# Optimization experiments

Measured on AMD Instinct MI355X. Metric: run time of the kernel, lower is better.

Reference implementation:

```python
import jax, jax.numpy as jnp
import numpy as np

N, E, HID, H, L, R = 20000, 160000, 512, 8, 4, 128
DK = HID // H
SCALE = 1.0 / np.sqrt(DK)
EPS = 1e-5


def setup_inputs() -> dict:
    key = jax.random.key(0)
    ks = jax.random.split(key, 24)
    p = lambda i, shape: jax.random.normal(ks[i], shape, jnp.float32) * 0.02
    return {
        'x': jax.random.normal(ks[0], (N, HID), jnp.float32),
        'relations': jax.random.randint(ks[1], (E,), 0, R),
        'src': jax.random.randint(ks[2], (E,), 0, N),
        'dst': jax.random.randint(ks[3], (E,), 0, N),
        'rel_embed': p(4, (R, HID)),
        'Wq': p(5, (L, HID, HID)), 'bq': jnp.zeros((L, HID), jnp.float32),
        'Wk': p(6, (L, HID, HID)), 'bk': jnp.zeros((L, HID), jnp.float32),
        'Wv': p(7, (L, HID, HID)), 'bv': jnp.zeros((L, HID), jnp.float32),
        'Wo': p(8, (L, HID, HID)), 'bo': jnp.zeros((L, HID), jnp.float32),
        'W1': p(9, (L, HID, 4 * HID)), 'b1': jnp.zeros((L, 4 * HID), jnp.float32),
        'W2': p(10, (L, 4 * HID, HID)), 'b2': jnp.zeros((L, HID), jnp.float32),
        'ln1_g': jnp.ones((L, HID), jnp.float32), 'ln1_b': jnp.zeros((L, HID), jnp.float32),
        'ln2_g': jnp.ones((L, HID), jnp.float32), 'ln2_b': jnp.zeros((L, HID), jnp.float32),
    }


def _ln(x, g, b):
    m = x.mean(-1, keepdims=True)
    v = jnp.square(x - m).mean(-1, keepdims=True)
    return (x - m) * jax.lax.rsqrt(v + EPS) * g + b


def _layer(x, rh, src, dst, Wq, bq, Wk, bk, Wv, bv, Wo, bo, W1, b1, W2, b2, g1, bb1, g2, bb2):
    # rh: (E, H, DK) per-edge relation features
    q = (x @ Wq + bq).reshape(N, H, DK)
    k = (x @ Wk + bk).reshape(N, H, DK)
    v = (x @ Wv + bv).reshape(N, H, DK)
    # edge score: ((k_src + r) . q_dst) / sqrt(d_k)   -> (E, H)
    score = jnp.einsum('ehd,ehd->eh', k[src] + rh, q[dst]) * SCALE
    # segment softmax over incoming edges of each dst node
    smax = jax.ops.segment_max(score, dst, num_segments=N)
    smax = jnp.where(jnp.isfinite(smax), smax, 0.0)  # nodes with no in-edges
    ex = jnp.exp(score - smax[dst])                   # (E, H)
    z = jax.ops.segment_sum(ex, dst, num_segments=N)  # (N, H)
    wv = jax.ops.segment_sum(ex[:, :, None] * (v[src] + rh), dst, num_segments=N)  # (N, H, DK)
    o = wv / (z[:, :, None] + 1e-9)
    o = o.reshape(N, HID) @ Wo + bo
    h = _ln(x + o, g1, bb1)
    ff = jax.nn.relu(h @ W1 + b1) @ W2 + b2
    return _ln(h + ff, g2, bb2)


def reference(x, relations, src, dst, rel_embed, Wq, bq, Wk, bk, Wv, bv, Wo, bo, W1, b1, W2, b2, ln1_g, ln1_b, ln2_g, ln2_b):
    lg_x = rel_embed[relations]            # (E, HID), shared across layers
    rh = lg_x.reshape(E, H, DK)
    for i in range(L):
        x = _layer(x, rh, src, dst, Wq[i], bq[i], Wk[i], bk[i], Wv[i], bv[i],
                   Wo[i], bo[i], W1[i], b1[i], W2[i], b2[i],
                   ln1_g[i], ln1_b[i], ln2_g[i], ln2_b[i])
    return x
```

## Files before the change

kernel.cpp:

```cpp
#include <hip/hip_runtime.h>
#include <cstdint>
#include <cstddef>

#define N_NODES 20000
#define N_EDGES 160000
#define HIDDEN  512
#define NHEAD   8
#define HDK     64
#define NLAYER  4
#define FFDIM   2048
#define ATT_SCALE 0.125f
#define S1C 262144
#define S2C 1048576
#define WLYR (4 * S1C + 2 * S2C)

typedef float  f4  __attribute__((ext_vector_type(4)));
typedef short  s8v __attribute__((ext_vector_type(8)));
typedef __bf16 b8v __attribute__((ext_vector_type(8)));

template <typename V>
__device__ inline auto mfma_try(V a, V b, f4 c, int)
    -> decltype(__builtin_amdgcn_mfma_f32_16x16x32_bf16(a, b, c, 0, 0, 0)) {
  return __builtin_amdgcn_mfma_f32_16x16x32_bf16(a, b, c, 0, 0, 0);
}
template <typename V>
__device__ inline f4 mfma_try(V a, V b, f4 c, long) {
  return __builtin_amdgcn_mfma_f32_16x16x32_bf16(
      __builtin_bit_cast(b8v, a), __builtin_bit_cast(b8v, b), c, 0, 0, 0);
}
__device__ inline f4 mfma_bf16(s8v a, s8v b, f4 c) { return mfma_try(a, b, c, 0); }

__device__ __forceinline__ unsigned short f2bf(float f) {
  unsigned u = __builtin_bit_cast(unsigned, f);
  u += 0x7FFFu + ((u >> 16) & 1u);
  return (unsigned short)(u >> 16);
}
__device__ __forceinline__ float bf2f(unsigned short u) {
  return __builtin_bit_cast(float, (unsigned)u << 16);
}

#define GLOAD_LDS16(gp, lp)                                                   \
  __builtin_amdgcn_global_load_lds(                                           \
      (const __attribute__((address_space(1))) void*)(gp),                    \
      (__attribute__((address_space(3))) void*)(lp), 16, 0, 0)

__global__ void cast8_kernel(const float* __restrict__ in, unsigned short* __restrict__ out, int n8) {
  int i = blockIdx.x * blockDim.x + threadIdx.x;
  if (i < n8) {
    f4 a = ((const f4*)in)[i * 2];
    f4 b = ((const f4*)in)[i * 2 + 1];
    s8v o;
#pragma unroll
    for (int j = 0; j < 4; ++j) {
      o[j]     = (short)f2bf(a[j]);
      o[j + 4] = (short)f2bf(b[j]);
    }
    ((s8v*)out)[i] = o;
  }
}

__global__ void weight_prep_kernel(const float* __restrict__ Wq, const float* __restrict__ Wk,
                                   const float* __restrict__ Wv, const float* __restrict__ Wo_,
                                   const float* __restrict__ W1, const float* __restrict__ W2,
                                   const float* __restrict__ bq, const float* __restrict__ bk,
                                   const float* __restrict__ bv,
                                   unsigned short* __restrict__ wAll, float* __restrict__ bqkvAll) {
  int l = blockIdx.x / 3078;
  int id = blockIdx.x % 3078;
  unsigned short* wqkv = wAll + (size_t)l * WLYR;
  unsigned short* wo = wqkv + 3 * S1C;
  unsigned short* w1 = wo + S1C;
  unsigned short* w2 = w1 + S2C;
  if (id >= 3072) {
    int i = (id - 3072) * 256 + threadIdx.y * 32 + threadIdx.x;
    float* bqkv = bqkvAll + l * 1536;
    if (i < 512) bqkv[i] = bq[l * 512 + i];
    else if (i < 1024) bqkv[i] = bk[l * 512 + i - 512];
    else if (i < 1536) bqkv[i] = bv[l * 512 + i - 1024];
    return;
  }
  const float* in; unsigned short* out; int K, N, bx, by;
  if (id < 1024) {
    int m = id >> 8, t = id & 255;
    in = ((m == 0) ? Wq : (m == 1) ? Wk : (m == 2) ? Wv : Wo_) + (size_t)l * S1C;
    out = (m == 3) ? wo : wqkv + m * S1C;
    K = 512; N = 512; bx = t & 15; by = t >> 4;
  } else if (id < 2048) {
    int t = id - 1024;
    in = W1 + (size_t)l * S2C; out = w1; K = 512; N = 2048; bx = t & 63; by = t >> 6;
  } else {
    int t = id - 2048;
    in = W2 + (size_t)l * S2C; out = w2; K = 2048; N = 512; bx = t & 15; by = t >> 4;
  }
  __shared__ float t32[32][33];
  int tx = threadIdx.x, ty = threadIdx.y;
  int n0 = bx * 32, k0 = by * 32;
  int Kc = K >> 3;
#pragma unroll
  for (int i = 0; i < 32; i += 8)
    t32[ty + i][tx] = in[(size_t)(k0 + ty + i) * N + n0 + tx];
  __syncthreads();
#pragma unroll
  for (int i = 0; i < 32; i += 8) {
    int n = n0 + ty + i, k = k0 + tx;
    size_t idx = ((size_t)(n >> 4) * Kc + (k >> 3)) * 128 + (n & 15) * 8 + (k & 7);
    out[idx] = f2bf(t32[tx][ty + i]);
  }
}

#define BM 128
#define BN 128
#define BK 64

template <bool OBF16, bool SPLITB>
__global__ __launch_bounds__(256, SPLITB ? 4 : 3) void gemm_bf16(
    const unsigned short* __restrict__ A, const unsigned short* __restrict__ Bt,
    const float* __restrict__ bias, void* __restrict__ Cp,
    int M, int K, int N, int relu) {
  __shared__ __align__(16) unsigned short As[8192];
  int tid = threadIdx.x;
  int wave = tid >> 6, lane = tid & 63;
  int quad = lane >> 4, l16 = lane & 15;
  int wm = (wave >> 1) * 64, wn = (wave & 1) * 64;

  int T = gridDim.x * gridDim.y;
  int i = blockIdx.y * gridDim.x + blockIdx.x;
  int C = T >> 3;
  int w = (i < (C << 3)) ? ((i & 7) * C + (i >> 3)) : i;
  int bx = w % gridDim.x, by = w / gridDim.x;
  int m0 = by * BM, n0 = bx * BN;

  f4 acc[4][4];
#pragma unroll
  for (int i2 = 0; i2 < 4; ++i2)
#pragma unroll
    for (int j = 0; j < 4; ++j) acc[i2][j] = (f4){0.f, 0.f, 0.f, 0.f};

  int rbase = wave * 8 + (lane >> 3);
  int q8 = (lane & 7) ^ ((lane >> 3) & 7);
  const unsigned short* aptr[4];
#pragma unroll
  for (int j = 0; j < 4; ++j) {
    int r = j * 32 + rbase;
    int gm = m0 + r; if (gm >= M) gm = M - 1;
    aptr[j] = A + (size_t)gm * K + q8 * 8;
  }

  int Kc = K >> 3;
  const unsigned short* bbase = Bt + quad * 128 + l16 * 8;
  size_t nioff[4];
#pragma unroll
  for (int i2 = 0; i2 < 4; ++i2)
    nioff[i2] = ((size_t)((n0 >> 4) + (wn >> 4) + i2) * Kc) * 128;

  int nk = K >> 6;
  for (int ks = 0; ks < nk; ++ks) {
#pragma unroll
    for (int j = 0; j < 4; ++j)
      GLOAD_LDS16(aptr[j], &As[j * 2048 + wave * 512]);

    if constexpr (SPLITB) {
      s8v bfr[4];
#pragma unroll
      for (int i2 = 0; i2 < 4; ++i2)
        bfr[i2] = *(const s8v*)(bbase + nioff[i2] + (size_t)ks * 1024);
#pragma unroll
      for (int j = 0; j < 4; ++j) aptr[j] += BK;
      __syncthreads();
      {
        s8v af[4];
#pragma unroll
        for (int i2 = 0; i2 < 4; ++i2) {
          int ra = wm + i2 * 16 + l16;
          af[i2] = *(const s8v*)(&As[ra * 64 + (((quad) ^ (ra & 7)) * 8)]);
        }
#pragma unroll
        for (int mi = 0; mi < 4; ++mi)
#pragma unroll
          for (int ni = 0; ni < 4; ++ni)
            acc[mi][ni] = mfma_bf16(af[mi], bfr[ni], acc[mi][ni]);
      }
#pragma unroll
      for (int i2 = 0; i2 < 4; ++i2)
        bfr[i2] = *(const s8v*)(bbase + nioff[i2] + (size_t)ks * 1024 + 512);
      {
        s8v af[4];
#pragma unroll
        for (int i2 = 0; i2 < 4; ++i2) {
          int ra = wm + i2 * 16 + l16;
          af[i2] = *(const s8v*)(&As[ra * 64 + (((4 | quad) ^ (ra & 7)) * 8)]);
        }
#pragma unroll
        for (int mi = 0; mi < 4; ++mi)
#pragma unroll
          for (int ni = 0; ni < 4; ++ni)
            acc[mi][ni] = mfma_bf16(af[mi], bfr[ni], acc[mi][ni]);
      }
      __syncthreads();
    } else {
      s8v bfr[2][4];
#pragma unroll
      for (int s = 0; s < 2; ++s)
#pragma unroll
        for (int i2 = 0; i2 < 4; ++i2)
          bfr[s][i2] = *(const s8v*)(bbase + nioff[i2] + (size_t)ks * 1024 + s * 512);
#pragma unroll
      for (int j = 0; j < 4; ++j) aptr[j] += BK;
      __syncthreads();
#pragma unroll
      for (int s = 0; s < 2; ++s) {
        s8v af[4];
#pragma unroll
        for (int i2 = 0; i2 < 4; ++i2) {
          int ra = wm + i2 * 16 + l16;
          af[i2] = *(const s8v*)(&As[ra * 64 + ((((s << 2) | quad) ^ (ra & 7)) * 8)]);
        }
#pragma unroll
        for (int mi = 0; mi < 4; ++mi)
#pragma unroll
          for (int ni = 0; ni < 4; ++ni)
            acc[mi][ni] = mfma_bf16(af[mi], bfr[s][ni], acc[mi][ni]);
      }
      __syncthreads();
    }
  }

  if constexpr (OBF16) {
    unsigned short* Cs = As + wave * 1088;
    float bvv[4];
#pragma unroll
    for (int ni = 0; ni < 4; ++ni) bvv[ni] = bias[n0 + wn + ni * 16 + l16];
    int row_l = lane >> 2, cg = lane & 3;
#pragma unroll
    for (int mi = 0; mi < 4; ++mi) {
#pragma unroll
      for (int ni = 0; ni < 4; ++ni) {
#pragma unroll
        for (int r = 0; r < 4; ++r) {
          float val = acc[mi][ni][r] + bvv[ni];
          if (relu) val = fmaxf(val, 0.f);
          Cs[(quad * 4 + r) * 68 + ni * 16 + l16] = f2bf(val);
        }
      }
      s8v v0 = *(const s8v*)(&Cs[row_l * 68 + cg * 16]);
      s8v v1 = *(const s8v*)(&Cs[row_l * 68 + cg * 16 + 8]);
      int grow = m0 + wm + mi * 16 + row_l;
      if (grow < M) {
        unsigned short* cp = (unsigned short*)Cp + (size_t)grow * N + n0 + wn + cg * 16;
        *(s8v*)cp = v0;
        *(s8v*)(cp + 8) = v1;
      }
    }
  } else {
#pragma unroll
    for (int ni = 0; ni < 4; ++ni) {
      int col = n0 + wn + ni * 16 + l16;
      float bv = bias[col];
#pragma unroll
      for (int mi = 0; mi < 4; ++mi) {
#pragma unroll
        for (int r = 0; r < 4; ++r) {
          int row = m0 + wm + mi * 16 + quad * 4 + r;
          if (row < M) {
            float val = acc[mi][ni][r] + bv;
            if (relu) val = fmaxf(val, 0.f);
            ((float*)Cp)[(size_t)row * N + col] = val;
          }
        }
      }
    }
  }
}

__global__ __launch_bounds__(256, 4) void gemm_sm(
    const unsigned short* __restrict__ A, const unsigned short* __restrict__ Bt,
    const float* __restrict__ bias, unsigned short* __restrict__ Cp,
    int M, int K, int N, int relu) {
  __shared__ __align__(16) unsigned short As[4096];
  int tid = threadIdx.x;
  int wave = tid >> 6, lane = tid & 63;
  int quad = lane >> 4, l16 = lane & 15;
  int wn = wave * 32;

  int T = gridDim.x * gridDim.y;
  int i = blockIdx.y * gridDim.x + blockIdx.x;
  int C = T >> 3;
  int w = (i < (C << 3)) ? ((i & 7) * C + (i >> 3)) : i;
  int bx = w % gridDim.x, by = w / gridDim.x;
  int m0 = by * 64, n0 = bx * BN;

  f4 acc[4][2];
#pragma unroll
  for (int i2 = 0; i2 < 4; ++i2)
#pragma unroll
    for (int j = 0; j < 2; ++j) acc[i2][j] = (f4){0.f, 0.f, 0.f, 0.f};

  int rbase = wave * 8 + (lane >> 3);
  int q8 = (lane & 7) ^ ((lane >> 3) & 7);
  const unsigned short* aptr[2];
#pragma unroll
  for (int j = 0; j < 2; ++j) {
    int r = j * 32 + rbase;
    int gm = m0 + r; if (gm >= M) gm = M - 1;
    aptr[j] = A + (size_t)gm * K + q8 * 8;
  }

  int Kc = K >> 3;
  const unsigned short* bbase = Bt + quad * 128 + l16 * 8;
  size_t nioff[2];
#pragma unroll
  for (int i2 = 0; i2 < 2; ++i2)
    nioff[i2] = ((size_t)((n0 >> 4) + (wn >> 4) + i2) * Kc) * 128;

  int nk = K >> 6;
  for (int ks = 0; ks < nk; ++ks) {
#pragma unroll
    for (int j = 0; j < 2; ++j)
      GLOAD_LDS16(aptr[j], &As[j * 2048 + wave * 512]);
    s8v bfr[2][2];
#pragma unroll
    for (int s = 0; s < 2; ++s)
#pragma unroll
      for (int i2 = 0; i2 < 2; ++i2)
        bfr[s][i2] = *(const s8v*)(bbase + nioff[i2] + (size_t)ks * 1024 + s * 512);
#pragma unroll
    for (int j = 0; j < 2; ++j) aptr[j] += BK;
    __syncthreads();
#pragma unroll
    for (int s = 0; s < 2; ++s) {
      s8v af[4];
#pragma unroll
      for (int i2 = 0; i2 < 4; ++i2) {
        int ra = i2 * 16 + l16;
        af[i2] = *(const s8v*)(&As[ra * 64 + ((((s << 2) | quad) ^ (ra & 7)) * 8)]);
      }
#pragma unroll
      for (int mi = 0; mi < 4; ++mi)
#pragma unroll
        for (int ni = 0; ni < 2; ++ni)
          acc[mi][ni] = mfma_bf16(af[mi], bfr[s][ni], acc[mi][ni]);
    }
    __syncthreads();
  }

  unsigned short* Cs = As + wave * 576;
  float bvv[2];
#pragma unroll
  for (int ni = 0; ni < 2; ++ni) bvv[ni] = bias[n0 + wn + ni * 16 + l16];
  int row_l = lane >> 2, cg = lane & 3;
#pragma unroll
  for (int mi = 0; mi < 4; ++mi) {
#pragma unroll
    for (int ni = 0; ni < 2; ++ni)
#pragma unroll
      for (int r = 0; r < 4; ++r) {
        float val = acc[mi][ni][r] + bvv[ni];
        if (relu) val = fmaxf(val, 0.f);
        Cs[(quad * 4 + r) * 36 + ni * 16 + l16] = f2bf(val);
      }
    s8v v0 = *(const s8v*)(&Cs[row_l * 36 + cg * 8]);
    int grow = m0 + mi * 16 + row_l;
    if (grow < M) {
      unsigned short* cp = Cp + (size_t)grow * N + n0 + wn + cg * 8;
      *(s8v*)cp = v0;
    }
  }
}

__global__ void hist_kernel(const int* __restrict__ dst, int* __restrict__ cnt, int E) {
  int e = blockIdx.x * blockDim.x + threadIdx.x;
  if (e < E) atomicAdd(&cnt[dst[e]], 1);
}

__global__ void scan_blk_kernel(const int* __restrict__ cnt, int* __restrict__ incl,
                                int* __restrict__ bsum, int n) {
  __shared__ int sh[1024];
  int tid = threadIdx.x;
  int gi = blockIdx.x * 1024 + tid;
  int v = (gi < n) ? cnt[gi] : 0;
  sh[tid] = v;
  __syncthreads();
  for (int s = 1; s < 1024; s <<= 1) {
    int t = (tid >= s) ? sh[tid - s] : 0;
    __syncthreads();
    sh[tid] += t;
    __syncthreads();
  }
  if (gi < n) incl[gi] = sh[tid];
  if (tid == 1023) bsum[blockIdx.x] = sh[1023];
}

__global__ void scan_mid_kernel(const int* __restrict__ bsum, int* __restrict__ boff, int nb) {
  if (threadIdx.x == 0 && blockIdx.x == 0) {
    int run = 0;
    for (int i = 0; i < nb; ++i) { boff[i] = run; run += bsum[i]; }
    boff[nb] = run;
  }
}

__global__ void scan_fix_kernel(const int* __restrict__ incl, const int* __restrict__ boff,
                                int* __restrict__ offs, int n) {
  int gi = blockIdx.x * 1024 + threadIdx.x;
  if (gi < n) offs[gi + 1] = boff[blockIdx.x] + incl[gi];
  if (gi == 0) offs[0] = 0;
}

__global__ void scatter_kernel(const int* __restrict__ dst, const int* __restrict__ src,
                               const int* __restrict__ relations, const int* __restrict__ offs,
                               int* __restrict__ cursor, int* __restrict__ esrc,
                               int* __restrict__ erel, int E) {
  int e = blockIdx.x * blockDim.x + threadIdx.x;
  if (e < E) {
    int d = dst[e];
    int pos = offs[d] + atomicAdd(&cursor[d], 1);
    esrc[pos] = src[e];
    erel[pos] = relations[e];
  }
}

#define ATT_LOAD(j, kx, vx, rx) do {                                          \
    int sj = __shfl(si_l, (j), 64);                                           \
    int rj = __shfl(ri_l, (j), 64);                                           \
    kx = *(const s8v*)(k + (size_t)sj * STR + base);                          \
    vx = *(const s8v*)(v + (size_t)sj * STR + base);                          \
    rx = *(const s8v*)(relb + (size_t)rj * HIDDEN + base);                    \
  } while (0)

#define ATT_STEP(kc, vc, rc) do {                                             \
    float rf[8], p = 0.f;                                                     \
    _Pragma("unroll") for (int jj = 0; jj < 8; ++jj) {                        \
      rf[jj] = bf2f((unsigned short)kc[jj]);                                  \
      float rr = bf2f((unsigned short)rc[jj]);                                \
      p += (rf[jj] + rr) * qf[jj];                                            \
      rf[jj] = rr;                                                            \
    }                                                                         \
    p += __shfl_xor(p, 1, 64);                                                \
    p += __shfl_xor(p, 2, 64);                                                \
    p += __shfl_xor(p, 4, 64);                                                \
    p *= ATT_SCALE;                                                           \
    float mn = fmaxf(m, p);                                                   \
    float a = __expf(m - mn);                                                 \
    float wgt = __expf(p - mn);                                               \
    z = z * a + wgt;                                                          \
    _Pragma("unroll") for (int jj = 0; jj < 8; ++jj)                          \
      acc[jj] = acc[jj] * a + wgt * (bf2f((unsigned short)vc[jj]) + rf[jj]);  \
    m = mn;                                                                   \
  } while (0)

__global__ void edge_attn_kernel(const unsigned short* __restrict__ q,
                                 const unsigned short* __restrict__ k,
                                 const unsigned short* __restrict__ v,
                                 const unsigned short* __restrict__ relb,
                                 const int* __restrict__ offs,
                                 const int* __restrict__ esrc,
                                 const int* __restrict__ erel,
                                 unsigned short* __restrict__ o, int Nn, int STR) {
  int wid = (blockIdx.x * blockDim.x + threadIdx.x) >> 6;
  int lane = threadIdx.x & 63;
  if (wid >= Nn) return;
  int base = (lane >> 3) * HDK + (lane & 7) * 8;

  s8v qv = *(const s8v*)(q + (size_t)wid * STR + base);
  float qf[8];
#pragma unroll
  for (int j = 0; j < 8; ++j) qf[j] = bf2f((unsigned short)qv[j]);

  int beg = offs[wid], end = offs[wid + 1];
  float m = -1e30f, z = 0.f;
  float acc[8];
#pragma unroll
  for (int j = 0; j < 8; ++j) acc[j] = 0.f;

  for (int cbeg = beg; cbeg < end; cbeg += 64) {
    int cn = end - cbeg; if (cn > 64) cn = 64;
    int e = cbeg + lane;
    int si_l = 0, ri_l = 0;
    if (e < end) { si_l = esrc[e]; ri_l = erel[e]; }
    s8v kA = {}, vA = {}, rA = {};
    s8v kB = {}, vB = {}, rB = {};
    s8v kC = {}, vC = {}, rC = {};
    if (cn > 0) ATT_LOAD(0, kA, vA, rA);
    if (cn > 1) ATT_LOAD(1, kB, vB, rB);
    if (cn > 2) ATT_LOAD(2, kC, vC, rC);
    int j = 0;
    for (; j + 5 < cn; j += 3) {
      ATT_STEP(kA, vA, rA); ATT_LOAD(j + 3, kA, vA, rA);
      ATT_STEP(kB, vB, rB); ATT_LOAD(j + 4, kB, vB, rB);
      ATT_STEP(kC, vC, rC); ATT_LOAD(j + 5, kC, vC, rC);
    }
    int r = cn - j;
    if (r >= 1) ATT_STEP(kA, vA, rA);
    if (r >= 4) ATT_LOAD(j + 3, kA, vA, rA);
    if (r >= 2) ATT_STEP(kB, vB, rB);
    if (r >= 5) ATT_LOAD(j + 4, kB, vB, rB);
    if (r >= 3) ATT_STEP(kC, vC, rC);
    if (r >= 4) ATT_STEP(kA, vA, rA);
    if (r >= 5) ATT_STEP(kB, vB, rB);
  }

  float rz = 1.f / (z + 1e-9f);
  s8v ov;
#pragma unroll
  for (int j = 0; j < 8; ++j) ov[j] = (short)f2bf(acc[j] * rz);
  *(s8v*)(o + (size_t)wid * HIDDEN + base) = ov;
}

template <bool WF32>
__global__ void ln_kernel(const unsigned short* __restrict__ xp, const unsigned short* __restrict__ y,
                          const float* __restrict__ g, const float* __restrict__ b,
                          float* __restrict__ outf, unsigned short* __restrict__ outb, int Nn) {
  int wid = (blockIdx.x * blockDim.x + threadIdx.x) >> 6;
  int lane = threadIdx.x & 63;
  if (wid >= Nn) return;
  int base = lane * 8;
  s8v xv = *(const s8v*)(xp + (size_t)wid * HIDDEN + base);
  s8v yv = *(const s8v*)(y + (size_t)wid * HIDDEN + base);
  float vals[8];
  float sum = 0.f;
#pragma unroll
  for (int j = 0; j < 8; ++j) {
    vals[j] = bf2f((unsigned short)xv[j]) + bf2f((unsigned short)yv[j]);
    sum += vals[j];
  }
#pragma unroll
  for (int off = 32; off; off >>= 1) sum += __shfl_xor(sum, off, 64);
  float mean = sum * (1.f / 512.f);
  float sq = 0.f;
#pragma unroll
  for (int j = 0; j < 8; ++j) { float d = vals[j] - mean; sq += d * d; }
#pragma unroll
  for (int off = 32; off; off >>= 1) sq += __shfl_xor(sq, off, 64);
  float rstd = rsqrtf(sq * (1.f / 512.f) + 1e-5f);
  f4 gv0 = *(const f4*)(g + base);
  f4 gv1 = *(const f4*)(g + base + 4);
  f4 bv0 = *(const f4*)(b + base);
  f4 bv1 = *(const f4*)(b + base + 4);
  float ov_f[8];
#pragma unroll
  for (int j = 0; j < 4; ++j) {
    ov_f[j]     = (vals[j]     - mean) * rstd * gv0[j] + bv0[j];
    ov_f[j + 4] = (vals[j + 4] - mean) * rstd * gv1[j] + bv1[j];
  }
  s8v ov;
#pragma unroll
  for (int j = 0; j < 8; ++j) ov[j] = (short)f2bf(ov_f[j]);
  *(s8v*)(outb + (size_t)wid * HIDDEN + base) = ov;
  if constexpr (WF32) {
    f4 o0, o1;
#pragma unroll
    for (int j = 0; j < 4; ++j) { o0[j] = ov_f[j]; o1[j] = ov_f[j + 4]; }
    *(f4*)(outf + (size_t)wid * HIDDEN + base) = o0;
    *(f4*)(outf + (size_t)wid * HIDDEN + base + 4) = o1;
  }
}

extern "C" void kernel_launch(void* const* d_in, const int* in_sizes, int n_in,
                              void* d_out, int out_size, void* d_ws, size_t ws_size,
                              hipStream_t stream) {
  const float* x0        = (const float*)d_in[0];
  const int*   relations = (const int*)d_in[1];
  const int*   src       = (const int*)d_in[2];
  const int*   dst       = (const int*)d_in[3];
  const float* rel_embed = (const float*)d_in[4];
  const float* Wq = (const float*)d_in[5];  const float* bq = (const float*)d_in[6];
  const float* Wk = (const float*)d_in[7];  const float* bk = (const float*)d_in[8];
  const float* Wv = (const float*)d_in[9];  const float* bv = (const float*)d_in[10];
  const float* Wo = (const float*)d_in[11]; const float* bo = (const float*)d_in[12];
  const float* W1 = (const float*)d_in[13]; const float* b1 = (const float*)d_in[14];
  const float* W2 = (const float*)d_in[15]; const float* b2 = (const float*)d_in[16];
  const float* g1  = (const float*)d_in[17]; const float* bb1 = (const float*)d_in[18];
  const float* g2  = (const float*)d_in[19]; const float* bb2 = (const float*)d_in[20];
  float* xout = (float*)d_out;

  const size_t S1 = S1C;
  const size_t S2 = S2C;
  const size_t NH = (size_t)N_NODES * HIDDEN;

  unsigned short* wAll = (unsigned short*)d_ws;
  float* bqkvAll = (float*)(wAll + (size_t)NLAYER * WLYR);
  unsigned short* arena = (unsigned short*)(bqkvAll + NLAYER * 1536);
  unsigned short* qkvb = arena;
  unsigned short* ob   = arena + 3 * NH;
  unsigned short* ff1  = arena;
  unsigned short* proj = arena;
  unsigned short* hbb = arena + 4 * NH;
  unsigned short* xb  = hbb + NH;
  unsigned short* projb = xb + NH;
  unsigned short* relb  = projb + NH;
  int* cnt    = (int*)(relb + 65536);
  int* offs   = cnt + N_NODES;
  int* cursor = offs + N_NODES + 1;
  int* esrc   = cursor + N_NODES;
  int* erel   = esrc + N_EDGES;
  int* sincl  = erel + N_EDGES;
  int* sbsum  = sincl + 20480;
  int* sboff  = sbsum + 32;

  hipMemsetAsync(cnt, 0, N_NODES * sizeof(int), stream);
  hipMemsetAsync(cursor, 0, N_NODES * sizeof(int), stream);
  hist_kernel<<<(N_EDGES + 255) / 256, 256, 0, stream>>>(dst, cnt, N_EDGES);
  const int NB = (N_NODES + 1023) / 1024;
  scan_blk_kernel<<<NB, 1024, 0, stream>>>(cnt, sincl, sbsum, N_NODES);
  scan_mid_kernel<<<1, 64, 0, stream>>>(sbsum, sboff, NB);
  scan_fix_kernel<<<NB, 1024, 0, stream>>>(sincl, sboff, offs, N_NODES);
  scatter_kernel<<<(N_EDGES + 255) / 256, 256, 0, stream>>>(dst, src, relations, offs, cursor, esrc, erel, N_EDGES);
  cast8_kernel<<<(int)((NH / 8 + 255) / 256), 256, 0, stream>>>(x0, xb, (int)(NH / 8));
  cast8_kernel<<<32, 256, 0, stream>>>(rel_embed, relb, 8192);
  dim3 tb(32, 8);
  weight_prep_kernel<<<NLAYER * 3078, tb, 0, stream>>>(Wq, Wk, Wv, Wo, W1, W2, bq, bk, bv,
                                                       wAll, bqkvAll);

  const int MBc = (N_NODES + BM - 1) / BM;
  const int MBs = (N_NODES + 63) / 64;

  for (int l = 0; l < NLAYER; ++l) {
    unsigned short* wqkv = wAll + (size_t)l * WLYR;
    unsigned short* wo = wqkv + 3 * S1;
    unsigned short* w1 = wo + S1;
    unsigned short* w2 = w1 + S2;
    float* bqkv = bqkvAll + l * 1536;
    gemm_bf16<true, true><<<dim3(12, MBc), 256, 0, stream>>>(xb, wqkv, bqkv, qkvb, N_NODES, 512, 1536, 0);
    edge_attn_kernel<<<(N_NODES + 3) / 4, 256, 0, stream>>>(qkvb, qkvb + 512, qkvb + 1024,
                                                            relb, offs, esrc, erel, ob, N_NODES, 1536);
    gemm_sm<<<dim3(4, MBs), 256, 0, stream>>>(ob, wo, bo + l * 512, proj, N_NODES, 512, 512, 0);
    ln_kernel<false><<<N_NODES / 4, 256, 0, stream>>>(xb, proj, g1 + l * 512, bb1 + l * 512, nullptr, hbb, N_NODES);
    gemm_bf16<true, true><<<dim3(16, MBc), 256, 0, stream>>>(hbb, w1, b1 + l * 2048, ff1, N_NODES, 512, 2048, 1);
    gemm_sm<<<dim3(4, MBs), 256, 0, stream>>>(ff1, w2, b2 + l * 512, projb, N_NODES, 2048, 512, 0);
    if (l == NLAYER - 1)
      ln_kernel<true><<<N_NODES / 4, 256, 0, stream>>>(hbb, projb, g2 + l * 512, bb2 + l * 512, xout, xb, N_NODES);
    else
      ln_kernel<false><<<N_NODES / 4, 256, 0, stream>>>(hbb, projb, g2 + l * 512, bb2 + l * 512, nullptr, xb, N_NODES);
  }
}
```

Baseline: 1.162 ms.

## Write FF1 output in MFMA fragment layout and add LDS-free FF2 GEMM

The FF1 GEMM epilogue now writes its bf16 output directly in the 16x8 fragment-tiled layout that the MFMA operands expect. A new gemm_ff2 kernel reads A and B fragments straight from global memory with no LDS staging or barriers in the K loop, then uses LDS only for the output epilogue. This removes the shared-memory staging and synchronisation from the K=2048 down-projection. The trade-off is reliance on cache hits for global loads, with no double buffering. The output ragged edge depends on M being a multiple of 16.

```diff
diff --git a/kernel.cpp b/kernel.cpp
--- a/kernel.cpp
+++ b/kernel.cpp
@@ -112,7 +112,7 @@
 #define BN 128
 #define BK 64
 
-template <bool OBF16, bool SPLITB>
+template <bool OBF16, bool SPLITB, bool OUTFRAG>
 __global__ __launch_bounds__(256, SPLITB ? 4 : 3) void gemm_bf16(
     const unsigned short* __restrict__ A, const unsigned short* __restrict__ Bt,
     const float* __restrict__ bias, void* __restrict__ Cp,
@@ -225,7 +225,34 @@
     }
   }
 
-  if constexpr (OBF16) {
+  if constexpr (OUTFRAG) {
+    unsigned short* Cs = As + wave * 1024;
+    float bvv[4];
+#pragma unroll
+    for (int ni = 0; ni < 4; ++ni) bvv[ni] = bias[n0 + wn + ni * 16 + l16];
+    int Kc2 = N >> 3;
+    int c0 = (n0 + wn) >> 3;
+#pragma unroll
+    for (int mi = 0; mi < 4; ++mi) {
+#pragma unroll
+      for (int ni = 0; ni < 4; ++ni)
+#pragma unroll
+        for (int r = 0; r < 4; ++r) {
+          float val = acc[mi][ni][r] + bvv[ni];
+          if (relu) val = fmaxf(val, 0.f);
+          Cs[(ni * 2 + (l16 >> 3)) * 128 + (quad * 4 + r) * 8 + (l16 & 7)] = f2bf(val);
+        }
+      s8v v0 = *(const s8v*)(&Cs[lane * 16]);
+      s8v v1 = *(const s8v*)(&Cs[lane * 16 + 8]);
+      int gb = m0 + wm + mi * 16;
+      if (gb < M) {
+        unsigned short* cp = (unsigned short*)Cp +
+            ((size_t)(gb >> 4) * Kc2 + c0) * 128 + lane * 16;
+        *(s8v*)cp = v0;
+        *(s8v*)(cp + 8) = v1;
+      }
+    }
+  } else if constexpr (OBF16) {
     unsigned short* Cs = As + wave * 1088;
     float bvv[4];
 #pragma unroll
@@ -356,6 +383,79 @@
       for (int r = 0; r < 4; ++r) {
         float val = acc[mi][ni][r] + bvv[ni];
         if (relu) val = fmaxf(val, 0.f);
+        Cs[(quad * 4 + r) * 36 + ni * 16 + l16] = f2bf(val);
+      }
+    s8v v0 = *(const s8v*)(&Cs[row_l * 36 + cg * 8]);
+    int grow = m0 + mi * 16 + row_l;
+    if (grow < M) {
+      unsigned short* cp = Cp + (size_t)grow * N + n0 + wn + cg * 8;
+      *(s8v*)cp = v0;
+    }
+  }
+}
+
+__global__ __launch_bounds__(256, 4) void gemm_ff2(
+    const unsigned short* __restrict__ Af, const unsigned short* __restrict__ Bt,
+    const float* __restrict__ bias, unsigned short* __restrict__ Cp,
+    int M, int K, int N) {
+  __shared__ __align__(16) unsigned short Cs_s[2304];
+  int tid = threadIdx.x;
+  int wave = tid >> 6, lane = tid & 63;
+  int quad = lane >> 4, l16 = lane & 15;
+  int wn = wave * 32;
+
+  int T = gridDim.x * gridDim.y;
+  int i = blockIdx.y * gridDim.x + blockIdx.x;
+  int C = T >> 3;
+  int w = (i < (C << 3)) ? ((i & 7) * C + (i >> 3)) : i;
+  int bx = w % gridDim.x, by = w / gridDim.x;
+  int m0 = by * 64, n0 = bx * 128;
+
+  f4 acc[4][2];
+#pragma unroll
+  for (int i2 = 0; i2 < 4; ++i2)
+#pragma unroll
+    for (int j = 0; j < 2; ++j) acc[i2][j] = (f4){0.f, 0.f, 0.f, 0.f};
+
+  int Kc = K >> 3;
+  const unsigned short* ab = Af + ((size_t)(m0 >> 4) * Kc) * 128 + quad * 128 + l16 * 8;
+  const unsigned short* bbase = Bt + quad * 128 + l16 * 8;
+  size_t nioff[2];
+#pragma unroll
+  for (int i2 = 0; i2 < 2; ++i2)
+    nioff[i2] = ((size_t)((n0 >> 4) + (wn >> 4) + i2) * Kc) * 128;
+
+  int nk = K >> 6;
+  for (int ks = 0; ks < nk; ++ks) {
+#pragma unroll
+    for (int s = 0; s < 2; ++s) {
+      s8v af[4], bf[2];
+#pragma unroll
+      for (int i2 = 0; i2 < 4; ++i2)
+        af[i2] = *(const s8v*)(ab + ((size_t)i2 * Kc) * 128 + (size_t)ks * 1024 + s * 512);
+#pragma unroll
+      for (int i2 = 0; i2 < 2; ++i2)
+        bf[i2] = *(const s8v*)(bbase + nioff[i2] + (size_t)ks * 1024 + s * 512);
+#pragma unroll
+      for (int mi = 0; mi < 4; ++mi)
+#pragma unroll
+        for (int ni = 0; ni < 2; ++ni)
+          acc[mi][ni] = mfma_bf16(af[mi], bf[ni], acc[mi][ni]);
+    }
+  }
+
+  unsigned short* Cs = Cs_s + wave * 576;
+  float bvv[2];
+#pragma unroll
+  for (int ni = 0; ni < 2; ++ni) bvv[ni] = bias[n0 + wn + ni * 16 + l16];
+  int row_l = lane >> 2, cg = lane & 3;
+#pragma unroll
+  for (int mi = 0; mi < 4; ++mi) {
+#pragma unroll
+    for (int ni = 0; ni < 2; ++ni)
+#pragma unroll
+      for (int r = 0; r < 4; ++r) {
+        float val = acc[mi][ni][r] + bvv[ni];
         Cs[(quad * 4 + r) * 36 + ni * 16 + l16] = f2bf(val);
       }
     s8v v0 = *(const s8v*)(&Cs[row_l * 36 + cg * 8]);
@@ -619,13 +719,13 @@
     unsigned short* w1 = wo + S1;
     unsigned short* w2 = w1 + S2;
     float* bqkv = bqkvAll + l * 1536;
-    gemm_bf16<true, true><<<dim3(12, MBc), 256, 0, stream>>>(xb, wqkv, bqkv, qkvb, N_NODES, 512, 1536, 0);
+    gemm_bf16<true, true, false><<<dim3(12, MBc), 256, 0, stream>>>(xb, wqkv, bqkv, qkvb, N_NODES, 512, 1536, 0);
     edge_attn_kernel<<<(N_NODES + 3) / 4, 256, 0, stream>>>(qkvb, qkvb + 512, qkvb + 1024,
                                                             relb, offs, esrc, erel, ob, N_NODES, 1536);
     gemm_sm<<<dim3(4, MBs), 256, 0, stream>>>(ob, wo, bo + l * 512, proj, N_NODES, 512, 512, 0);
     ln_kernel<false><<<N_NODES / 4, 256, 0, stream>>>(xb, proj, g1 + l * 512, bb1 + l * 512, nullptr, hbb, N_NODES);
-    gemm_bf16<true, true><<<dim3(16, MBc), 256, 0, stream>>>(hbb, w1, b1 + l * 2048, ff1, N_NODES, 512, 2048, 1);
-    gemm_sm<<<dim3(4, MBs), 256, 0, stream>>>(ff1, w2, b2 + l * 512, projb, N_NODES, 2048, 512, 0);
+    gemm_bf16<true, true, true><<<dim3(16, MBc), 256, 0, stream>>>(hbb, w1, b1 + l * 2048, ff1, N_NODES, 512, 2048, 1);
+    gemm_ff2<<<dim3(4, MBs), 256, 0, stream>>>(ff1, w2, b2 + l * 512, projb, N_NODES, 2048, 512);
     if (l == NLAYER - 1)
       ln_kernel<true><<<N_NODES / 4, 256, 0, stream>>>(hbb, projb, g2 + l * 512, bb2 + l * 512, xout, xb, N_NODES);
     else
```

After: 1.275 ms. 1.1x slower.
